# Kernel tuning notes

Measured on AMD Instinct MI355X. Metric: run time of the kernel, lower is better.

Reference implementation:

```python
import jax, jax.numpy as jnp
import numpy as np

MIN_V, MAX_V = 1e-7, 10.0
POWER = 2.0
N_NODES = 200000


def _hyper_layer(H, edges, W, b):
    """One HyperTensorGraphConvolution layer (full-neighborhood branch).

    H: [N, d] node signals; edges: [E, S] node indices per hyperedge.
    For each (edge, node_i): power-mean over the other S-1 nodes of the edge,
    divided by (S-1), accumulated onto node_i; then row-normalize and linear.
    """
    N, d = H.shape
    E, S = edges.shape
    H = jnp.clip(H, MIN_V, MAX_V)
    P = H ** POWER                                   # [N, d]
    g = P[edges]                                     # [E, S, d] gather
    edge_sum = g.sum(axis=1, keepdims=True)          # [E, 1, d]
    neigh_mean = (edge_sum - g) / (S - 1)            # exclude self, /(len(nodes)-1)
    contrib = neigh_mean ** (1.0 / POWER)            # [E, S, d]
    add = jax.ops.segment_sum(contrib.reshape(E * S, d),
                              edges.reshape(-1), num_segments=N)
    new_signal = H + add
    # row-normalize (rowsum > 0 because H >= 1e-7)
    rowsum = new_signal.sum(axis=1)
    r_inv = jnp.where(jnp.isfinite(1.0 / rowsum), 1.0 / rowsum, 0.0)
    AH = new_signal * r_inv[:, None]
    return AH @ W + b


def setup_inputs() -> dict:
    key = jax.random.key(0)
    k1, k2, k3, k4, k5, k6 = jax.random.split(key, 6)
    d, h, c = 128, 16, 40
    H = jax.random.uniform(k1, (N_NODES, d), dtype=jnp.float32)
    edges = jax.random.randint(k2, (40000, 16), 0, N_NODES, dtype=jnp.int64)
    std1 = 1.0 / np.sqrt(h)
    std2 = 1.0 / np.sqrt(c)
    W1 = jax.random.uniform(k3, (d, h), jnp.float32, -std1, std1)
    b1 = jax.random.uniform(k4, (h,), jnp.float32, -std1, std1)
    W2 = jax.random.uniform(k5, (h, c), jnp.float32, -std2, std2)
    b2 = jax.random.uniform(k6, (c,), jnp.float32, -std2, std2)
    return {"H": H, "W1": W1, "b1": b1, "W2": W2, "b2": b2, "edges": edges}


def reference(H, W1, b1, W2, b2, edges):
    # layer 1 + relu (dropout is identity in eval mode)
    x = jax.nn.relu(_hyper_layer(H, edges, W1, b1))
    # layer 2
    return _hyper_layer(x, edges, W2, b2)
```

## Files before the change

### kernel.cpp

```cpp
#include <hip/hip_runtime.h>

#define MIN_V 1e-7f
#define MAX_V 10.0f
#define INV15 (1.0f/15.0f)
#define CAP 32

typedef _Float16 half2v __attribute__((ext_vector_type(2)));
typedef _Float16 half4v __attribute__((ext_vector_type(4)));
typedef _Float16 half8v __attribute__((ext_vector_type(8)));

static __device__ __forceinline__ float clipv(float v){
    return fminf(fmaxf(v, MIN_V), MAX_V);
}
static __device__ __forceinline__ float rsqrt_arg(float v){
    return __builtin_amdgcn_sqrtf(fmaxf(v, 0.f));
}

__global__ __launch_bounds__(256) void ch_build(
    const float* __restrict__ H, _Float16* __restrict__ CH, int total8,
    const int* __restrict__ edges, int* __restrict__ cnt,
    unsigned short* __restrict__ lists, int total){
    int i = blockIdx.x*256 + threadIdx.x;
    if (i < total8){
        const float4* p = (const float4*)(H + (size_t)i*8);
        float4 a = p[0], b = p[1];
        half8v o;
        o[0]=(_Float16)clipv(a.x); o[1]=(_Float16)clipv(a.y);
        o[2]=(_Float16)clipv(a.z); o[3]=(_Float16)clipv(a.w);
        o[4]=(_Float16)clipv(b.x); o[5]=(_Float16)clipv(b.y);
        o[6]=(_Float16)clipv(b.z); o[7]=(_Float16)clipv(b.w);
        *(half8v*)(CH + (size_t)i*8) = o;
    }
    if (i < total){
        int node = edges[i];
        int p = atomicAdd(&cnt[node], 1);
        if (p < CAP) lists[(size_t)node*CAP + p] = (unsigned short)(i >> 4);
    }
}

__global__ __launch_bounds__(256) void es_l1(const _Float16* __restrict__ CH,
                                             const int* __restrict__ edges,
                                             _Float16* __restrict__ ES1s, int E){
    int wave = threadIdx.x >> 6, lane = threadIdx.x & 63;
    int e = blockIdx.x*4 + wave;
    if (e >= E) return;
    int rid = edges[(size_t)e*16 + (lane & 15)];
    float s0 = 0.f, s1 = 0.f;
    #pragma unroll
    for (int s=0;s<16;++s){
        int idx = __shfl(rid, s, 64);
        half2v v = *(const half2v*)(CH + (size_t)idx*128 + lane*2);
        float f0 = (float)v[0], f1 = (float)v[1];
        s0 += f0*f0; s1 += f1*f1;
    }
    half2v o; o[0] = (_Float16)(s0*INV15); o[1] = (_Float16)(s1*INV15);
    *(half2v*)(ES1s + (size_t)e*128 + lane*2) = o;
}

__global__ __launch_bounds__(256) void gather_l1(
    const _Float16* __restrict__ CH, const _Float16* __restrict__ ES1s,
    const int* __restrict__ cnt, const unsigned short* __restrict__ lists,
    _Float16* __restrict__ NEW1, int N){
    int t = blockIdx.x*256 + threadIdx.x;
    int n = t >> 5;
    if (n >= N) return;
    int k32 = t & 31;
    int dq = k32 * 4;

    int myid = (int)lists[(size_t)n*CAP + k32];
    int len = cnt[n]; if (len > CAP) len = CAP;

    half4v hv = *(const half4v*)(CH + (size_t)n*128 + dq);
    float h0=(float)hv[0], h1=(float)hv[1], h2=(float)hv[2], h3=(float)hv[3];
    float p0=h0*h0*INV15, p1=h1*h1*INV15, p2=h2*h2*INV15, p3=h3*h3*INV15;

    float a0=0.f, a1=0.f, a2=0.f, a3=0.f;
    for (int k0=0;k0<len;k0+=4){
        int e0 = __shfl(myid, k0+0, 32);
        int e1 = __shfl(myid, k0+1, 32);
        int e2 = __shfl(myid, k0+2, 32);
        int e3 = __shfl(myid, k0+3, 32);
        half4v v0 = *(const half4v*)(ES1s + (size_t)e0*128 + dq);
        half4v v1 = *(const half4v*)(ES1s + (size_t)e1*128 + dq);
        half4v v2 = *(const half4v*)(ES1s + (size_t)e2*128 + dq);
        half4v v3 = *(const half4v*)(ES1s + (size_t)e3*128 + dq);
        a0 += rsqrt_arg((float)v0[0] - p0);
        a1 += rsqrt_arg((float)v0[1] - p1);
        a2 += rsqrt_arg((float)v0[2] - p2);
        a3 += rsqrt_arg((float)v0[3] - p3);
        bool m1 = (k0+1 < len), m2 = (k0+2 < len), m3 = (k0+3 < len);
        a0 += m1 ? rsqrt_arg((float)v1[0] - p0) : 0.f;
        a1 += m1 ? rsqrt_arg((float)v1[1] - p1) : 0.f;
        a2 += m1 ? rsqrt_arg((float)v1[2] - p2) : 0.f;
        a3 += m1 ? rsqrt_arg((float)v1[3] - p3) : 0.f;
        a0 += m2 ? rsqrt_arg((float)v2[0] - p0) : 0.f;
        a1 += m2 ? rsqrt_arg((float)v2[1] - p1) : 0.f;
        a2 += m2 ? rsqrt_arg((float)v2[2] - p2) : 0.f;
        a3 += m2 ? rsqrt_arg((float)v2[3] - p3) : 0.f;
        a0 += m3 ? rsqrt_arg((float)v3[0] - p0) : 0.f;
        a1 += m3 ? rsqrt_arg((float)v3[1] - p1) : 0.f;
        a2 += m3 ? rsqrt_arg((float)v3[2] - p2) : 0.f;
        a3 += m3 ? rsqrt_arg((float)v3[3] - p3) : 0.f;
    }
    half4v o;
    o[0]=(_Float16)(h0+a0); o[1]=(_Float16)(h1+a1);
    o[2]=(_Float16)(h2+a2); o[3]=(_Float16)(h3+a3);
    *(half4v*)(NEW1 + (size_t)n*128 + dq) = o;
}

__global__ __launch_bounds__(256) void gemm_l1(
    const _Float16* __restrict__ NEW1, const float* __restrict__ W1,
    const float* __restrict__ b1, _Float16* __restrict__ X, int N){
    int wave = threadIdx.x >> 6, lane = threadIdx.x & 63;
    int q = lane >> 4, h = lane & 15;
    float w[32];
    #pragma unroll
    for (int i=0;i<32;++i) w[i] = W1[(q*32+i)*16 + h];
    float bv = b1[h];

    for (int n = blockIdx.x*4 + wave; n < N; n += gridDim.x*4){
        const half8v* row = (const half8v*)(NEW1 + (size_t)n*128 + q*32);
        float acc = 0.f, rs = 0.f;
        #pragma unroll
        for (int j=0;j<4;++j){
            half8v v = row[j];
            #pragma unroll
            for (int u=0;u<8;++u){
                float f = (float)v[u];
                acc += f * w[j*8+u];
                rs  += f;
            }
        }
        acc += __shfl_xor(acc, 16, 64);
        rs  += __shfl_xor(rs , 16, 64);
        acc += __shfl_xor(acc, 32, 64);
        rs  += __shfl_xor(rs , 32, 64);
        if (q == 0){
            float o = acc * __builtin_amdgcn_rcpf(rs) + bv;
            X[(size_t)n*16 + h] = (_Float16)fmaxf(o, 0.f);
        }
    }
}

__global__ __launch_bounds__(256) void es_l2(const _Float16* __restrict__ X,
                                             const int* __restrict__ edges,
                                             _Float16* __restrict__ ES2s, int E){
    int t = blockIdx.x*256 + threadIdx.x;
    int e = t >> 3, dd2 = (t & 7)*2;
    if (e >= E) return;
    const int* row = edges + (size_t)e*16;
    float s0 = 0.f, s1 = 0.f;
    #pragma unroll
    for (int s=0;s<16;++s){
        half2v v = *(const half2v*)(X + (size_t)row[s]*16 + dd2);
        float f0 = clipv((float)v[0]), f1 = clipv((float)v[1]);
        s0 += f0*f0; s1 += f1*f1;
    }
    half2v o; o[0]=(_Float16)(s0*INV15); o[1]=(_Float16)(s1*INV15);
    *(half2v*)(ES2s + (size_t)e*16 + dd2) = o;
}

__global__ __launch_bounds__(256) void node_l2(
    const _Float16* __restrict__ X, const _Float16* __restrict__ ES2s,
    const int* __restrict__ cnt, const unsigned short* __restrict__ lists,
    const float* __restrict__ W2, const float* __restrict__ b2,
    float* __restrict__ out, int N){
    __shared__ float sW[640];
    __shared__ float sb[40];
    for (int i=threadIdx.x;i<640;i+=256) sW[i] = W2[i];
    if (threadIdx.x < 40) sb[threadIdx.x] = b2[threadIdx.x];
    __syncthreads();
    int n = blockIdx.x*256 + threadIdx.x;
    if (n >= N) return;
    float xc[16], ps[16], ad[16];
    const half8v* xr = (const half8v*)(X + (size_t)n*16);
    half8v x0 = xr[0], x1 = xr[1];
    #pragma unroll
    for (int d=0;d<8;++d){
        float v = clipv((float)x0[d]);
        xc[d]=v; ps[d]=v*v*INV15; ad[d]=0.f;
    }
    #pragma unroll
    for (int d=0;d<8;++d){
        float v = clipv((float)x1[d]);
        xc[8+d]=v; ps[8+d]=v*v*INV15; ad[8+d]=0.f;
    }
    int len = cnt[n]; if (len > CAP) len = CAP;
    const unsigned short* lrow = lists + (size_t)n*CAP;
    for (int k0=0;k0<len;k0+=2){
        int e0 = lrow[k0];
        int e1 = (k0+1 < len) ? lrow[k0+1] : e0;
        bool m1 = (k0+1 < len);
        const half8v* r0 = (const half8v*)(ES2s + (size_t)e0*16);
        const half8v* r1 = (const half8v*)(ES2s + (size_t)e1*16);
        half8v ea0 = r0[0], eb0 = r0[1];
        half8v ea1 = r1[0], eb1 = r1[1];
        #pragma unroll
        for (int d=0;d<8;++d){
            ad[d]   += rsqrt_arg((float)ea0[d] - ps[d]);
            ad[8+d] += rsqrt_arg((float)eb0[d] - ps[8+d]);
        }
        #pragma unroll
        for (int d=0;d<8;++d){
            ad[d]   += m1 ? rsqrt_arg((float)ea1[d] - ps[d])   : 0.f;
            ad[8+d] += m1 ? rsqrt_arg((float)eb1[d] - ps[8+d]) : 0.f;
        }
    }
    float rs = 0.f;
    float nw[16];
    #pragma unroll
    for (int d=0;d<16;++d){ nw[d] = xc[d] + ad[d]; rs += nw[d]; }
    float rinv = __builtin_amdgcn_rcpf(rs);
    float acc[40];
    #pragma unroll
    for (int c=0;c<40;++c) acc[c] = 0.f;
    #pragma unroll
    for (int d=0;d<16;++d){
        float v = nw[d];
        #pragma unroll
        for (int c=0;c<40;++c) acc[c] += v * sW[d*40+c];
    }
    float4 ob[10];
    #pragma unroll
    for (int c=0;c<40;++c) ((float*)ob)[c] = rinv*acc[c] + sb[c];
    float4* op = (float4*)(out + (size_t)n*40);
    #pragma unroll
    for (int j=0;j<10;++j) op[j] = ob[j];
}

extern "C" void kernel_launch(void* const* d_in, const int* in_sizes, int n_in,
                              void* d_out, int out_size, void* d_ws, size_t ws_size,
                              hipStream_t stream){
    (void)n_in; (void)out_size; (void)ws_size;
    const float* H  = (const float*)d_in[0];
    const float* W1 = (const float*)d_in[1];
    const float* b1 = (const float*)d_in[2];
    const float* W2 = (const float*)d_in[3];
    const float* b2 = (const float*)d_in[4];
    const int* edges = (const int*)d_in[5];
    float* out = (float*)d_out;

    const int N = in_sizes[0] / 128;
    const int E = in_sizes[5] / 16;
    const int total = E * 16;
    const int total8 = N * 128 / 8;

    char* ws = (char*)d_ws;
    size_t off = 0;
    _Float16* CH   = (_Float16*)(ws + off);
    _Float16* X    = (_Float16*)(ws + off);
    _Float16* ES2s = (_Float16*)(ws + off + (size_t)N*16*sizeof(_Float16));
    off += (size_t)N*128*sizeof(_Float16);
    _Float16* ES1s = (_Float16*)(ws + off); off += (size_t)E*128*sizeof(_Float16);
    _Float16* NEW1 = (_Float16*)(ws + off); off += (size_t)N*128*sizeof(_Float16);
    int* cnt = (int*)(ws + off); off += (size_t)N*sizeof(int);
    unsigned short* lists = (unsigned short*)(ws + off);
    off += (size_t)N*CAP*sizeof(unsigned short);

    hipMemsetAsync(cnt, 0, (size_t)N*sizeof(int), stream);
    ch_build<<<(total8+255)/256, 256, 0, stream>>>(H, CH, total8, edges, cnt, lists, total);
    es_l1<<<(E+3)/4, 256, 0, stream>>>(CH, edges, ES1s, E);
    gather_l1<<<(N*32+255)/256, 256, 0, stream>>>(CH, ES1s, cnt, lists, NEW1, N);
    gemm_l1<<<2048, 256, 0, stream>>>(NEW1, W1, b1, X, N);
    es_l2<<<(E*8+255)/256, 256, 0, stream>>>(X, edges, ES2s, E);
    node_l2<<<(N+255)/256, 256, 0, stream>>>(X, ES2s, cnt, lists, W2, b2, out, N);
}
```

Baseline: 215.6 us.

## Fuse layer-1 gather with row-normalize GEMM via shared memory; split CH conversion from list build

Merges the layer-1 neighbor gather and the 128x16 linear/row-normalization into one kernel. Each block computes 8 node rows of the new signal in fp32, stages them in padded shared memory, and then applies W1 and the row sum directly, so the fp16 NEW1 intermediate is never written to or read back from global memory. The clip/fp16 conversion of H is moved into a grid-stride kernel, and the edge-list atomic build becomes its own kernel, adding one launch. In exchange, W1 is reloaded into registers by every block (25k blocks instead of 2048), and the fused kernel adds a __syncthreads.

```diff
diff --git a/kernel.cpp b/kernel.cpp
--- a/kernel.cpp
+++ b/kernel.cpp
@@ -16,12 +16,10 @@
     return __builtin_amdgcn_sqrtf(fmaxf(v, 0.f));
 }
 
-__global__ __launch_bounds__(256) void ch_build(
-    const float* __restrict__ H, _Float16* __restrict__ CH, int total8,
-    const int* __restrict__ edges, int* __restrict__ cnt,
-    unsigned short* __restrict__ lists, int total){
-    int i = blockIdx.x*256 + threadIdx.x;
-    if (i < total8){
+__global__ __launch_bounds__(256) void ch_stream(const float* __restrict__ H,
+                                                 _Float16* __restrict__ CH, int total8){
+    int stride = gridDim.x*256;
+    for (int i = blockIdx.x*256 + threadIdx.x; i < total8; i += stride){
         const float4* p = (const float4*)(H + (size_t)i*8);
         float4 a = p[0], b = p[1];
         half8v o;
@@ -31,11 +29,15 @@
         o[6]=(_Float16)clipv(b.z); o[7]=(_Float16)clipv(b.w);
         *(half8v*)(CH + (size_t)i*8) = o;
     }
-    if (i < total){
-        int node = edges[i];
-        int p = atomicAdd(&cnt[node], 1);
-        if (p < CAP) lists[(size_t)node*CAP + p] = (unsigned short)(i >> 4);
-    }
+}
+
+__global__ void build_lists(const int* __restrict__ edges, int* __restrict__ cnt,
+                            unsigned short* __restrict__ lists, int total){
+    int i = blockIdx.x*256 + threadIdx.x;
+    if (i >= total) return;
+    int node = edges[i];
+    int p = atomicAdd(&cnt[node], 1);
+    if (p < CAP) lists[(size_t)node*CAP + p] = (unsigned short)(i >> 4);
 }
 
 __global__ __launch_bounds__(256) void es_l1(const _Float16* __restrict__ CH,
@@ -57,79 +59,81 @@
     *(half2v*)(ES1s + (size_t)e*128 + lane*2) = o;
 }
 
-__global__ __launch_bounds__(256) void gather_l1(
+__global__ __launch_bounds__(256) void fused_l1(
     const _Float16* __restrict__ CH, const _Float16* __restrict__ ES1s,
     const int* __restrict__ cnt, const unsigned short* __restrict__ lists,
-    _Float16* __restrict__ NEW1, int N){
-    int t = blockIdx.x*256 + threadIdx.x;
-    int n = t >> 5;
-    if (n >= N) return;
-    int k32 = t & 31;
-    int dq = k32 * 4;
-
-    int myid = (int)lists[(size_t)n*CAP + k32];
-    int len = cnt[n]; if (len > CAP) len = CAP;
-
-    half4v hv = *(const half4v*)(CH + (size_t)n*128 + dq);
-    float h0=(float)hv[0], h1=(float)hv[1], h2=(float)hv[2], h3=(float)hv[3];
-    float p0=h0*h0*INV15, p1=h1*h1*INV15, p2=h2*h2*INV15, p3=h3*h3*INV15;
-
-    float a0=0.f, a1=0.f, a2=0.f, a3=0.f;
-    for (int k0=0;k0<len;k0+=4){
-        int e0 = __shfl(myid, k0+0, 32);
-        int e1 = __shfl(myid, k0+1, 32);
-        int e2 = __shfl(myid, k0+2, 32);
-        int e3 = __shfl(myid, k0+3, 32);
-        half4v v0 = *(const half4v*)(ES1s + (size_t)e0*128 + dq);
-        half4v v1 = *(const half4v*)(ES1s + (size_t)e1*128 + dq);
-        half4v v2 = *(const half4v*)(ES1s + (size_t)e2*128 + dq);
-        half4v v3 = *(const half4v*)(ES1s + (size_t)e3*128 + dq);
-        a0 += rsqrt_arg((float)v0[0] - p0);
-        a1 += rsqrt_arg((float)v0[1] - p1);
-        a2 += rsqrt_arg((float)v0[2] - p2);
-        a3 += rsqrt_arg((float)v0[3] - p3);
-        bool m1 = (k0+1 < len), m2 = (k0+2 < len), m3 = (k0+3 < len);
-        a0 += m1 ? rsqrt_arg((float)v1[0] - p0) : 0.f;
-        a1 += m1 ? rsqrt_arg((float)v1[1] - p1) : 0.f;
-        a2 += m1 ? rsqrt_arg((float)v1[2] - p2) : 0.f;
-        a3 += m1 ? rsqrt_arg((float)v1[3] - p3) : 0.f;
-        a0 += m2 ? rsqrt_arg((float)v2[0] - p0) : 0.f;
-        a1 += m2 ? rsqrt_arg((float)v2[1] - p1) : 0.f;
-        a2 += m2 ? rsqrt_arg((float)v2[2] - p2) : 0.f;
-        a3 += m2 ? rsqrt_arg((float)v2[3] - p3) : 0.f;
-        a0 += m3 ? rsqrt_arg((float)v3[0] - p0) : 0.f;
-        a1 += m3 ? rsqrt_arg((float)v3[1] - p1) : 0.f;
-        a2 += m3 ? rsqrt_arg((float)v3[2] - p2) : 0.f;
-        a3 += m3 ? rsqrt_arg((float)v3[3] - p3) : 0.f;
-    }
-    half4v o;
-    o[0]=(_Float16)(h0+a0); o[1]=(_Float16)(h1+a1);
-    o[2]=(_Float16)(h2+a2); o[3]=(_Float16)(h3+a3);
-    *(half4v*)(NEW1 + (size_t)n*128 + dq) = o;
-}
-
-__global__ __launch_bounds__(256) void gemm_l1(
-    const _Float16* __restrict__ NEW1, const float* __restrict__ W1,
-    const float* __restrict__ b1, _Float16* __restrict__ X, int N){
-    int wave = threadIdx.x >> 6, lane = threadIdx.x & 63;
+    const float* __restrict__ W1, const float* __restrict__ b1,
+    _Float16* __restrict__ X, int N){
+    __shared__ float snw[8*144];
+    int tid = threadIdx.x;
+    int wave = tid >> 6, lane = tid & 63;
+
     int q = lane >> 4, h = lane & 15;
     float w[32];
     #pragma unroll
     for (int i=0;i<32;++i) w[i] = W1[(q*32+i)*16 + h];
     float bv = b1[h];
 
-    for (int n = blockIdx.x*4 + wave; n < N; n += gridDim.x*4){
-        const half8v* row = (const half8v*)(NEW1 + (size_t)n*128 + q*32);
+    int hw = tid >> 5;
+    int k32 = tid & 31;
+    int dq = k32 * 4;
+
+    int nb = blockIdx.x * 8;
+
+    int n = nb + hw;
+    if (n < N){
+        int myid = (int)lists[(size_t)n*CAP + k32];
+        int len = cnt[n]; if (len > CAP) len = CAP;
+
+        half4v hv = *(const half4v*)(CH + (size_t)n*128 + dq);
+        float h0=(float)hv[0], h1=(float)hv[1], h2=(float)hv[2], h3=(float)hv[3];
+        float p0=h0*h0*INV15, p1=h1*h1*INV15, p2=h2*h2*INV15, p3=h3*h3*INV15;
+
+        float a0=0.f, a1=0.f, a2=0.f, a3=0.f;
+        for (int k0=0;k0<len;k0+=4){
+            int e0 = __shfl(myid, k0+0, 32);
+            int e1 = __shfl(myid, k0+1, 32);
+            int e2 = __shfl(myid, k0+2, 32);
+            int e3 = __shfl(myid, k0+3, 32);
+            half4v v0 = *(const half4v*)(ES1s + (size_t)e0*128 + dq);
+            half4v v1 = *(const half4v*)(ES1s + (size_t)e1*128 + dq);
+            half4v v2 = *(const half4v*)(ES1s + (size_t)e2*128 + dq);
+            half4v v3 = *(const half4v*)(ES1s + (size_t)e3*128 + dq);
+            a0 += rsqrt_arg((float)v0[0] - p0);
+            a1 += rsqrt_arg((float)v0[1] - p1);
+            a2 += rsqrt_arg((float)v0[2] - p2);
+            a3 += rsqrt_arg((float)v0[3] - p3);
+            bool m1 = (k0+1 < len), m2 = (k0+2 < len), m3 = (k0+3 < len);
+            a0 += m1 ? rsqrt_arg((float)v1[0] - p0) : 0.f;
+            a1 += m1 ? rsqrt_arg((float)v1[1] - p1) : 0.f;
+            a2 += m1 ? rsqrt_arg((float)v1[2] - p2) : 0.f;
+            a3 += m1 ? rsqrt_arg((float)v1[3] - p3) : 0.f;
+            a0 += m2 ? rsqrt_arg((float)v2[0] - p0) : 0.f;
+            a1 += m2 ? rsqrt_arg((float)v2[1] - p1) : 0.f;
+            a2 += m2 ? rsqrt_arg((float)v2[2] - p2) : 0.f;
+            a3 += m2 ? rsqrt_arg((float)v2[3] - p3) : 0.f;
+            a0 += m3 ? rsqrt_arg((float)v3[0] - p0) : 0.f;
+            a1 += m3 ? rsqrt_arg((float)v3[1] - p1) : 0.f;
+            a2 += m3 ? rsqrt_arg((float)v3[2] - p2) : 0.f;
+            a3 += m3 ? rsqrt_arg((float)v3[3] - p3) : 0.f;
+        }
+        float4 wv;
+        wv.x = h0+a0; wv.y = h1+a1; wv.z = h2+a2; wv.w = h3+a3;
+        *(float4*)&snw[hw*144 + (k32>>3)*36 + (k32&7)*4] = wv;
+    }
+    __syncthreads();
+
+    #pragma unroll
+    for (int r=0;r<2;++r){
+        int nl = wave*2 + r;
+        int n2 = nb + nl;
+        if (n2 >= N) continue;
         float acc = 0.f, rs = 0.f;
         #pragma unroll
-        for (int j=0;j<4;++j){
-            half8v v = row[j];
-            #pragma unroll
-            for (int u=0;u<8;++u){
-                float f = (float)v[u];
-                acc += f * w[j*8+u];
-                rs  += f;
-            }
+        for (int j=0;j<8;++j){
+            float4 v = *(const float4*)&snw[nl*144 + q*36 + j*4];
+            acc += v.x*w[j*4+0] + v.y*w[j*4+1] + v.z*w[j*4+2] + v.w*w[j*4+3];
+            rs  += v.x + v.y + v.z + v.w;
         }
         acc += __shfl_xor(acc, 16, 64);
         rs  += __shfl_xor(rs , 16, 64);
@@ -137,7 +141,7 @@
         rs  += __shfl_xor(rs , 32, 64);
         if (q == 0){
             float o = acc * __builtin_amdgcn_rcpf(rs) + bv;
-            X[(size_t)n*16 + h] = (_Float16)fmaxf(o, 0.f);
+            X[(size_t)n2*16 + h] = (_Float16)fmaxf(o, 0.f);
         }
     }
 }
@@ -252,16 +256,15 @@
     _Float16* ES2s = (_Float16*)(ws + off + (size_t)N*16*sizeof(_Float16));
     off += (size_t)N*128*sizeof(_Float16);
     _Float16* ES1s = (_Float16*)(ws + off); off += (size_t)E*128*sizeof(_Float16);
-    _Float16* NEW1 = (_Float16*)(ws + off); off += (size_t)N*128*sizeof(_Float16);
     int* cnt = (int*)(ws + off); off += (size_t)N*sizeof(int);
     unsigned short* lists = (unsigned short*)(ws + off);
     off += (size_t)N*CAP*sizeof(unsigned short);
 
     hipMemsetAsync(cnt, 0, (size_t)N*sizeof(int), stream);
-    ch_build<<<(total8+255)/256, 256, 0, stream>>>(H, CH, total8, edges, cnt, lists, total);
+    ch_stream<<<2048, 256, 0, stream>>>(H, CH, total8);
+    build_lists<<<(total+255)/256, 256, 0, stream>>>(edges, cnt, lists, total);
     es_l1<<<(E+3)/4, 256, 0, stream>>>(CH, edges, ES1s, E);
-    gather_l1<<<(N*32+255)/256, 256, 0, stream>>>(CH, ES1s, cnt, lists, NEW1, N);
-    gemm_l1<<<2048, 256, 0, stream>>>(NEW1, W1, b1, X, N);
+    fused_l1<<<(N+7)/8, 256, 0, stream>>>(CH, ES1s, cnt, lists, W1, b1, X, N);
     es_l2<<<(E*8+255)/256, 256, 0, stream>>>(X, edges, ES2s, E);
     node_l2<<<(N+255)/256, 256, 0, stream>>>(X, ES2s, cnt, lists, W2, b2, out, N);
 }
```

Result: faster. 197.0 us (-8.6%).
